# Optimization experiments

Measured on AMD Instinct MI355X. Metric: run time of the kernel, lower is better.

## Reference

```python
import jax, jax.numpy as jnp
import numpy as np

EPS = 1e-12  # F.normalize eps


def setup_inputs() -> dict:
    key = jax.random.key(0)
    k1, k2 = jax.random.split(key)
    bs, d = 8192, 128
    data = jax.random.normal(k1, (bs, d), dtype=jnp.float32)
    label = jax.random.randint(k2, (bs, 1), 0, 2, dtype=jnp.int64)
    scale = jnp.asarray(np.log(1.0 / 0.07), dtype=jnp.float32)  # learned temperature param
    return {"data": data, "scale": scale, "label": label}


def reference(data, scale, label):
    bs = data.shape[0]
    # L2-normalize rows (F.normalize semantics with eps clamp)
    norm = jnp.maximum(jnp.linalg.norm(data, axis=-1, keepdims=True), EPS)
    x = data / norm
    logits = (x @ x.T) * jnp.exp(scale)  # [bs, bs]
    # Vectorized equivalent of the python double loop: binary same-class matrix
    sim = (label == label.T).astype(logits.dtype)  # [bs, bs]
    q = jax.nn.softmax(sim / jnp.sum(sim, axis=-1, keepdims=True), axis=-1)
    p = jax.nn.log_softmax(logits, axis=-1)
    log_q = jnp.log(q)  # q > 0 always (softmax output)
    # F.kl_div(p, q, 'batchmean') = sum(q * (log q - p)) / bs
    loss1 = jnp.sum(q * (log_q - p)) / bs
    # F.kl_div(q.log(), p.exp(), 'batchmean') = sum(exp(p) * (p - log q)) / bs
    loss2 = jnp.sum(jnp.exp(p) * (p - log_q)) / bs
    return (loss1 + loss2) * 0.5
```

## Files before the change

### kernel.cpp

```cpp
#include <hip/hip_runtime.h>
#include <stdint.h>

#define BS 8192
#define DD 128
#define SPLIT 16

typedef __attribute__((ext_vector_type(8))) short short8;
typedef __attribute__((ext_vector_type(4))) float float4v;

__device__ __forceinline__ float bf2f(short s) {
  union { unsigned u; float f; } c;
  c.u = ((unsigned)(unsigned short)s) << 16;
  return c.f;
}
__device__ __forceinline__ short f2bf(float f) {
  union { float f; unsigned u; } c; c.f = f;
  unsigned u = c.u + 0x7FFFu + ((c.u >> 16) & 1u);
  return (short)(u >> 16);
}

__global__ __launch_bounds__(256) void k_norm(const float* __restrict__ data,
                                              const int* __restrict__ label,
                                              unsigned int* __restrict__ xnb32,
                                              float* __restrict__ xnf,
                                              float* __restrict__ gh,
                                              int* __restrict__ cnt,
                                              float* __restrict__ Zr,
                                              float* __restrict__ Ur,
                                              float* __restrict__ Vr,
                                              float* __restrict__ out) {
  __shared__ float sh[256];
  __shared__ int shc[2];
  int tid = threadIdx.x, wave = tid >> 6, lane = tid & 63;
  if (tid < 2) shc[tid] = 0;
  sh[tid] = 0.f;
  if (tid < 32) {
    int row = blockIdx.x * 32 + tid;
    Zr[row] = 0.f; Ur[row] = 0.f; Vr[row] = 0.f;
  }
  if (blockIdx.x == 0 && tid == 0) out[0] = 0.f;
  __syncthreads();
  float a00 = 0.f, a01 = 0.f, a10 = 0.f, a11 = 0.f;
  int c0 = 0, c1 = 0;
  int rbase = blockIdx.x * 32 + wave * 8;
  for (int r = 0; r < 8; ++r) {
    int row = rbase + r;
    float2 v = *(const float2*)&data[row * DD + lane * 2];
    float ss = v.x * v.x + v.y * v.y;
    for (int off = 32; off; off >>= 1) ss += __shfl_xor(ss, off);
    float rn = 1.f / fmaxf(sqrtf(ss), 1e-12f);
    float x0 = v.x * rn, x1 = v.y * rn;
    *(float2*)&xnf[row * DD + lane * 2] = make_float2(x0, x1);
    unsigned int pk = (unsigned int)(unsigned short)f2bf(x0) |
                      ((unsigned int)(unsigned short)f2bf(x1) << 16);
    xnb32[row * 64 + lane] = pk;
    int lab = label[row];
    if (lab == 0) { a00 += x0; a01 += x1; c0++; }
    else          { a10 += x0; a11 += x1; c1++; }
  }
  atomicAdd(&sh[2 * lane], a00);
  atomicAdd(&sh[2 * lane + 1], a01);
  atomicAdd(&sh[128 + 2 * lane], a10);
  atomicAdd(&sh[128 + 2 * lane + 1], a11);
  if (lane == 0) { atomicAdd(&shc[0], c0); atomicAdd(&shc[1], c1); }
  __syncthreads();
  atomicAdd(&gh[tid], sh[tid]);
  if (tid < 2) atomicAdd(&cnt[tid], shc[tid]);
}

__global__ __launch_bounds__(256) void k_main(const unsigned short* __restrict__ xnb,
                                              const int* __restrict__ label,
                                              const float* __restrict__ scale,
                                              float* __restrict__ Zr,
                                              float* __restrict__ Ur,
                                              float* __restrict__ Vr) {
  __shared__ short tile[64 * DD];
  int tid = threadIdx.x, wave = tid >> 6, lane = tid & 63;
  int quad = lane >> 4, col = lane & 15;
  int rb = blockIdx.x / SPLIT, sl = blockIdx.x % SPLIT;
  float se = __expf(scale[0]);

  short8 afrag[2][4];
  int labI[2][4];
#pragma unroll
  for (int s = 0; s < 2; ++s) {
    int arow = rb * 128 + s * 64 + wave * 16 + col;
    const short* ap = (const short*)xnb + (size_t)arow * DD;
#pragma unroll
    for (int t = 0; t < 4; ++t) {
      short8 a = *(const short8*)(ap + t * 32 + quad * 8);
#pragma unroll
      for (int i = 0; i < 8; ++i) a[i] = f2bf(bf2f(a[i]) * se);
      afrag[s][t] = a;
    }
#pragma unroll
    for (int r = 0; r < 4; ++r)
      labI[s][r] = label[rb * 128 + s * 64 + wave * 16 + quad * 4 + r];
  }

  float Z[2][4] = {}, U[2][4] = {}, V0[2][4] = {};

  const char* srcbase = (const char*)xnb;
  int rowloc = tid >> 4;
  int swz = (tid & 15) ^ rowloc;
  for (int j0 = sl * (BS / SPLIT); j0 < (sl + 1) * (BS / SPLIT); j0 += 64) {
    __syncthreads();
    char* dst = ((char*)tile) + tid * 16;
#pragma unroll
    for (int p = 0; p < 4; ++p) {
      const char* src = srcbase + (size_t)(j0 + p * 16 + rowloc) * 256 + swz * 16;
      __builtin_amdgcn_global_load_lds(
          (const __attribute__((address_space(1))) void*)(uintptr_t)src,
          (__attribute__((address_space(3))) void*)(uintptr_t)(dst + p * 4096), 16, 0, 0);
    }
    __syncthreads();
#pragma unroll
    for (int jo = 0; jo < 4; ++jo) {
      int jc = j0 + jo * 16 + col;
      float m0 = (label[jc] == 0) ? 1.f : 0.f;
      float4v c0 = {0.f, 0.f, 0.f, 0.f}, c1 = {0.f, 0.f, 0.f, 0.f};
      const short* bp = tile + (jo * 16 + col) * DD;
#pragma unroll
      for (int t = 0; t < 4; ++t) {
        short8 b = *(const short8*)(bp + ((t * 4 + quad) ^ col) * 8);
        c0 = __builtin_amdgcn_mfma_f32_16x16x32_bf16(afrag[0][t], b, c0, 0, 0, 0);
        c1 = __builtin_amdgcn_mfma_f32_16x16x32_bf16(afrag[1][t], b, c1, 0, 0, 0);
      }
#pragma unroll
      for (int r = 0; r < 4; ++r) {
        float l0 = c0[r], e0 = __expf(l0);
        Z[0][r] += e0; U[0][r] += e0 * l0; V0[0][r] += m0 * e0;
        float l1 = c1[r], e1 = __expf(l1);
        Z[1][r] += e1; U[1][r] += e1 * l1; V0[1][r] += m0 * e1;
      }
    }
  }
#pragma unroll
  for (int s = 0; s < 2; ++s)
#pragma unroll
    for (int r = 0; r < 4; ++r)
#pragma unroll
      for (int off = 1; off < 16; off <<= 1) {
        Z[s][r] += __shfl_xor(Z[s][r], off);
        U[s][r] += __shfl_xor(U[s][r], off);
        V0[s][r] += __shfl_xor(V0[s][r], off);
      }
  if (col == 0) {
#pragma unroll
    for (int s = 0; s < 2; ++s)
#pragma unroll
      for (int r = 0; r < 4; ++r) {
        int row = rb * 128 + s * 64 + wave * 16 + quad * 4 + r;
        float v = (labI[s][r] == 0) ? V0[s][r] : (Z[s][r] - V0[s][r]);
        atomicAdd(&Zr[row], Z[s][r]);
        atomicAdd(&Ur[row], U[s][r]);
        atomicAdd(&Vr[row], v);
      }
  }
}

__global__ __launch_bounds__(256) void k_final(const float* __restrict__ xnf,
                                               const int* __restrict__ label,
                                               const float* __restrict__ scale,
                                               const float* __restrict__ gh,
                                               const int* __restrict__ cnt,
                                               const float* __restrict__ Zr,
                                               const float* __restrict__ Ur,
                                               const float* __restrict__ Vr,
                                               float* __restrict__ out) {
  __shared__ float bsum[4];
  int tid = threadIdx.x, wave = tid >> 6, lane = tid & 63;
  float se = __expf(scale[0]);
  float h0a = gh[2 * lane], h0b = gh[2 * lane + 1];
  float h1a = gh[128 + 2 * lane], h1b = gh[128 + 2 * lane + 1];
  float ga = h0a + h1a, gb = h0b + h1b;
  float c0 = (float)cnt[0], c1 = (float)cnt[1];
  float local = 0.f;
  int rbase = blockIdx.x * 32 + wave * 8;
  for (int r = 0; r < 8; ++r) {
    int row = rbase + r;
    float2 x = *(const float2*)&xnf[row * DD + lane * 2];
    int lab = label[row];
    float sg = x.x * ga + x.y * gb;
    float sh_ = (lab == 0) ? (x.x * h0a + x.y * h0b) : (x.x * h1a + x.y * h1b);
    for (int off = 32; off; off >>= 1) {
      sg += __shfl_xor(sg, off);
      sh_ += __shfl_xor(sh_, off);
    }
    if (lane == 0) {
      float cc = (lab == 0) ? c0 : c1;
      float a = __expf(1.f / cc);
      float Zq = cc * a + ((float)BS - cc);
      float S = se * sg, T = se * sh_;
      float Z = Zr[row], U = Ur[row], V = Vr[row];
      local += a / Zq - (S + (a - 1.f) * T) / Zq + U / Z - V / (cc * Z);
    }
  }
  if (lane == 0) bsum[wave] = local;
  __syncthreads();
  if (tid == 0) {
    float s = bsum[0] + bsum[1] + bsum[2] + bsum[3];
    atomicAdd(out, s * (0.5f / (float)BS));
  }
}

extern "C" void kernel_launch(void* const* d_in, const int* in_sizes, int n_in,
                              void* d_out, int out_size, void* d_ws, size_t ws_size,
                              hipStream_t stream) {
  const float* data = (const float*)d_in[0];
  const float* scale = (const float*)d_in[1];
  const int* label = (const int*)d_in[2];
  char* ws = (char*)d_ws;
  unsigned short* xnb = (unsigned short*)ws;
  unsigned int* xnb32 = (unsigned int*)ws;
  float* xnf = (float*)(ws + 2097152);
  float* Zr = (float*)(ws + 6291456);
  float* Ur = (float*)(ws + 6324224);
  float* Vr = (float*)(ws + 6356992);
  float* gh = (float*)(ws + 6389760);
  int* cnt = (int*)(ws + 6390784);

  hipMemsetAsync(ws + 6389760, 0, 1032, stream);

  k_norm<<<256, 256, 0, stream>>>(data, label, xnb32, xnf, gh, cnt, Zr, Ur, Vr,
                                  (float*)d_out);
  k_main<<<64 * SPLIT, 256, 0, stream>>>(xnb, label, scale, Zr, Ur, Vr);
  k_final<<<256, 256, 0, stream>>>(xnf, label, scale, gh, cnt, Zr, Ur, Vr, (float*)d_out);
}
```

Measured before the change: 125.0 us.

## Load B fragments directly from global, use exp2, and precompute label masks

The main loop no longer stages 64-row tiles into LDS with block-wide barriers. Each wave now reads its B fragments straight from global memory, 16 columns at a time with a 2x unroll, relying on L1/L2 to serve the same rows to all four waves. The exponent moves to base 2 by folding log2(e) into the prescaled A fragments, and the U sum is rescaled by ln2 at the end. A float same-class mask per column is now precomputed in the normalisation kernel instead of comparing labels in the inner loop. This drops the barrier and LDS cost, but each wave now issues its own redundant global loads and depends on cache hit rates.

```diff
diff --git a/kernel.cpp b/kernel.cpp
--- a/kernel.cpp
+++ b/kernel.cpp
@@ -7,6 +7,12 @@
 
 typedef __attribute__((ext_vector_type(8))) short short8;
 typedef __attribute__((ext_vector_type(4))) float float4v;
+
+#if __has_builtin(__builtin_amdgcn_exp2f)
+#define EXP2(x) __builtin_amdgcn_exp2f(x)
+#else
+#define EXP2(x) exp2f(x)
+#endif
 
 __device__ __forceinline__ float bf2f(short s) {
   union { unsigned u; float f; } c;
@@ -28,6 +34,7 @@
                                               float* __restrict__ Zr,
                                               float* __restrict__ Ur,
                                               float* __restrict__ Vr,
+                                              float* __restrict__ mf,
                                               float* __restrict__ out) {
   __shared__ float sh[256];
   __shared__ int shc[2];
@@ -37,6 +44,7 @@
   if (tid < 32) {
     int row = blockIdx.x * 32 + tid;
     Zr[row] = 0.f; Ur[row] = 0.f; Vr[row] = 0.f;
+    mf[row] = (label[row] == 0) ? 1.f : 0.f;
   }
   if (blockIdx.x == 0 && tid == 0) out[0] = 0.f;
   __syncthreads();
@@ -70,15 +78,15 @@
 
 __global__ __launch_bounds__(256) void k_main(const unsigned short* __restrict__ xnb,
                                               const int* __restrict__ label,
+                                              const float* __restrict__ mf,
                                               const float* __restrict__ scale,
                                               float* __restrict__ Zr,
                                               float* __restrict__ Ur,
                                               float* __restrict__ Vr) {
-  __shared__ short tile[64 * DD];
   int tid = threadIdx.x, wave = tid >> 6, lane = tid & 63;
   int quad = lane >> 4, col = lane & 15;
   int rb = blockIdx.x / SPLIT, sl = blockIdx.x % SPLIT;
-  float se = __expf(scale[0]);
+  float se2 = __expf(scale[0]) * 1.4426950408889634f;
 
   short8 afrag[2][4];
   int labI[2][4];
@@ -90,7 +98,7 @@
     for (int t = 0; t < 4; ++t) {
       short8 a = *(const short8*)(ap + t * 32 + quad * 8);
 #pragma unroll
-      for (int i = 0; i < 8; ++i) a[i] = f2bf(bf2f(a[i]) * se);
+      for (int i = 0; i < 8; ++i) a[i] = f2bf(bf2f(a[i]) * se2);
       afrag[s][t] = a;
     }
 #pragma unroll
@@ -100,39 +108,31 @@
 
   float Z[2][4] = {}, U[2][4] = {}, V0[2][4] = {};
 
-  const char* srcbase = (const char*)xnb;
-  int rowloc = tid >> 4;
-  int swz = (tid & 15) ^ rowloc;
-  for (int j0 = sl * (BS / SPLIT); j0 < (sl + 1) * (BS / SPLIT); j0 += 64) {
-    __syncthreads();
-    char* dst = ((char*)tile) + tid * 16;
-#pragma unroll
-    for (int p = 0; p < 4; ++p) {
-      const char* src = srcbase + (size_t)(j0 + p * 16 + rowloc) * 256 + swz * 16;
-      __builtin_amdgcn_global_load_lds(
-          (const __attribute__((address_space(1))) void*)(uintptr_t)src,
-          (__attribute__((address_space(3))) void*)(uintptr_t)(dst + p * 4096), 16, 0, 0);
-    }
-    __syncthreads();
-#pragma unroll
-    for (int jo = 0; jo < 4; ++jo) {
-      int jc = j0 + jo * 16 + col;
-      float m0 = (label[jc] == 0) ? 1.f : 0.f;
-      float4v c0 = {0.f, 0.f, 0.f, 0.f}, c1 = {0.f, 0.f, 0.f, 0.f};
-      const short* bp = tile + (jo * 16 + col) * DD;
-#pragma unroll
-      for (int t = 0; t < 4; ++t) {
-        short8 b = *(const short8*)(bp + ((t * 4 + quad) ^ col) * 8);
-        c0 = __builtin_amdgcn_mfma_f32_16x16x32_bf16(afrag[0][t], b, c0, 0, 0, 0);
-        c1 = __builtin_amdgcn_mfma_f32_16x16x32_bf16(afrag[1][t], b, c1, 0, 0, 0);
-      }
-#pragma unroll
-      for (int r = 0; r < 4; ++r) {
-        float l0 = c0[r], e0 = __expf(l0);
-        Z[0][r] += e0; U[0][r] += e0 * l0; V0[0][r] += m0 * e0;
-        float l1 = c1[r], e1 = __expf(l1);
-        Z[1][r] += e1; U[1][r] += e1 * l1; V0[1][r] += m0 * e1;
-      }
+  const short* xs = (const short*)xnb;
+#pragma unroll 2
+  for (int j0 = sl * (BS / SPLIT); j0 < (sl + 1) * (BS / SPLIT); j0 += 16) {
+    int jc = j0 + col;
+    float m0 = mf[jc];
+    const short* bp = xs + (size_t)jc * DD + quad * 8;
+    short8 b0 = *(const short8*)(bp);
+    short8 b1 = *(const short8*)(bp + 32);
+    short8 b2 = *(const short8*)(bp + 64);
+    short8 b3 = *(const short8*)(bp + 96);
+    float4v c0 = {0.f, 0.f, 0.f, 0.f}, c1 = {0.f, 0.f, 0.f, 0.f};
+    c0 = __builtin_amdgcn_mfma_f32_16x16x32_bf16(afrag[0][0], b0, c0, 0, 0, 0);
+    c1 = __builtin_amdgcn_mfma_f32_16x16x32_bf16(afrag[1][0], b0, c1, 0, 0, 0);
+    c0 = __builtin_amdgcn_mfma_f32_16x16x32_bf16(afrag[0][1], b1, c0, 0, 0, 0);
+    c1 = __builtin_amdgcn_mfma_f32_16x16x32_bf16(afrag[1][1], b1, c1, 0, 0, 0);
+    c0 = __builtin_amdgcn_mfma_f32_16x16x32_bf16(afrag[0][2], b2, c0, 0, 0, 0);
+    c1 = __builtin_amdgcn_mfma_f32_16x16x32_bf16(afrag[1][2], b2, c1, 0, 0, 0);
+    c0 = __builtin_amdgcn_mfma_f32_16x16x32_bf16(afrag[0][3], b3, c0, 0, 0, 0);
+    c1 = __builtin_amdgcn_mfma_f32_16x16x32_bf16(afrag[1][3], b3, c1, 0, 0, 0);
+#pragma unroll
+    for (int r = 0; r < 4; ++r) {
+      float l0 = c0[r], e0 = EXP2(l0);
+      Z[0][r] += e0; U[0][r] += e0 * l0; V0[0][r] += m0 * e0;
+      float l1 = c1[r], e1 = EXP2(l1);
+      Z[1][r] += e1; U[1][r] += e1 * l1; V0[1][r] += m0 * e1;
     }
   }
 #pragma unroll
@@ -153,7 +153,7 @@
         int row = rb * 128 + s * 64 + wave * 16 + quad * 4 + r;
         float v = (labI[s][r] == 0) ? V0[s][r] : (Z[s][r] - V0[s][r]);
         atomicAdd(&Zr[row], Z[s][r]);
-        atomicAdd(&Ur[row], U[s][r]);
+        atomicAdd(&Ur[row], U[s][r] * 0.6931471805599453f);
         atomicAdd(&Vr[row], v);
       }
   }
@@ -219,11 +219,12 @@
   float* Vr = (float*)(ws + 6356992);
   float* gh = (float*)(ws + 6389760);
   int* cnt = (int*)(ws + 6390784);
+  float* mf = (float*)(ws + 6390800);
 
   hipMemsetAsync(ws + 6389760, 0, 1032, stream);
 
-  k_norm<<<256, 256, 0, stream>>>(data, label, xnb32, xnf, gh, cnt, Zr, Ur, Vr,
+  k_norm<<<256, 256, 0, stream>>>(data, label, xnb32, xnf, gh, cnt, Zr, Ur, Vr, mf,
                                   (float*)d_out);
-  k_main<<<64 * SPLIT, 256, 0, stream>>>(xnb, label, scale, Zr, Ur, Vr);
+  k_main<<<64 * SPLIT, 256, 0, stream>>>(xnb, label, mf, scale, Zr, Ur, Vr);
   k_final<<<256, 256, 0, stream>>>(xnf, label, scale, gh, cnt, Zr, Ur, Vr, (float*)d_out);
 }
```

New measurement: 155.5 us. 24.4% more time.

## Double-buffer LDS tiles, use exp2 with pre-scaled logits, precompute label mask

Applied to the files above, without the earlier changes.

Splits the B-tile LDS buffer in two so the global-to-LDS load of the next 64-column tile overlaps the MFMA/exp work on the current one, removing one barrier per tile. It also folds log2(e) into the scaled A fragments so the inner loop uses a native exp2, rescaling U by ln2 at the end. The per-column label compare becomes a precomputed float mask written by k_norm. In exchange, LDS use doubles (32 KB per block), which may lower occupancy, and there is one redundant wrap-around prefetch at the end of the loop.

```diff
diff --git a/kernel.cpp b/kernel.cpp
--- a/kernel.cpp
+++ b/kernel.cpp
@@ -7,6 +7,12 @@
 
 typedef __attribute__((ext_vector_type(8))) short short8;
 typedef __attribute__((ext_vector_type(4))) float float4v;
+
+#if __has_builtin(__builtin_amdgcn_exp2f)
+#define EXP2(x) __builtin_amdgcn_exp2f(x)
+#else
+#define EXP2(x) exp2f(x)
+#endif
 
 __device__ __forceinline__ float bf2f(short s) {
   union { unsigned u; float f; } c;
@@ -28,6 +34,7 @@
                                               float* __restrict__ Zr,
                                               float* __restrict__ Ur,
                                               float* __restrict__ Vr,
+                                              float* __restrict__ mf,
                                               float* __restrict__ out) {
   __shared__ float sh[256];
   __shared__ int shc[2];
@@ -37,6 +44,7 @@
   if (tid < 32) {
     int row = blockIdx.x * 32 + tid;
     Zr[row] = 0.f; Ur[row] = 0.f; Vr[row] = 0.f;
+    mf[row] = (label[row] == 0) ? 1.f : 0.f;
   }
   if (blockIdx.x == 0 && tid == 0) out[0] = 0.f;
   __syncthreads();
@@ -68,17 +76,59 @@
   if (tid < 2) atomicAdd(&cnt[tid], shc[tid]);
 }
 
+__device__ __forceinline__ void stage_tile(const char* srcbase, int j0,
+                                           char* dstbase, int tid) {
+  int rowloc = tid >> 4;
+  int swz = (tid & 15) ^ rowloc;
+  char* dst = dstbase + tid * 16;
+#pragma unroll
+  for (int p = 0; p < 4; ++p) {
+    const char* src = srcbase + (size_t)(j0 + p * 16 + rowloc) * 256 + swz * 16;
+    __builtin_amdgcn_global_load_lds(
+        (const __attribute__((address_space(1))) void*)(uintptr_t)src,
+        (__attribute__((address_space(3))) void*)(uintptr_t)(dst + p * 4096), 16, 0, 0);
+  }
+}
+
+__device__ __forceinline__ void consume_tile(const short* __restrict__ tile, int j0,
+                                             const float* __restrict__ mf,
+                                             const short8 afrag[2][4], int quad, int col,
+                                             float Z[2][4], float U[2][4], float V0[2][4]) {
+#pragma unroll
+  for (int jo = 0; jo < 4; ++jo) {
+    int jc = j0 + jo * 16 + col;
+    float m0 = mf[jc];
+    float4v c0 = {0.f, 0.f, 0.f, 0.f}, c1 = {0.f, 0.f, 0.f, 0.f};
+    const short* bp = tile + (jo * 16 + col) * DD;
+#pragma unroll
+    for (int t = 0; t < 4; ++t) {
+      short8 b = *(const short8*)(bp + ((t * 4 + quad) ^ col) * 8);
+      c0 = __builtin_amdgcn_mfma_f32_16x16x32_bf16(afrag[0][t], b, c0, 0, 0, 0);
+      c1 = __builtin_amdgcn_mfma_f32_16x16x32_bf16(afrag[1][t], b, c1, 0, 0, 0);
+    }
+#pragma unroll
+    for (int r = 0; r < 4; ++r) {
+      float l0 = c0[r], e0 = EXP2(l0);
+      Z[0][r] += e0; U[0][r] += e0 * l0; V0[0][r] += m0 * e0;
+      float l1 = c1[r], e1 = EXP2(l1);
+      Z[1][r] += e1; U[1][r] += e1 * l1; V0[1][r] += m0 * e1;
+    }
+  }
+}
+
 __global__ __launch_bounds__(256) void k_main(const unsigned short* __restrict__ xnb,
                                               const int* __restrict__ label,
+                                              const float* __restrict__ mf,
                                               const float* __restrict__ scale,
                                               float* __restrict__ Zr,
                                               float* __restrict__ Ur,
                                               float* __restrict__ Vr) {
-  __shared__ short tile[64 * DD];
+  __shared__ short tileA[64 * DD];
+  __shared__ short tileB[64 * DD];
   int tid = threadIdx.x, wave = tid >> 6, lane = tid & 63;
   int quad = lane >> 4, col = lane & 15;
   int rb = blockIdx.x / SPLIT, sl = blockIdx.x % SPLIT;
-  float se = __expf(scale[0]);
+  float se2 = __expf(scale[0]) * 1.4426950408889634f;
 
   short8 afrag[2][4];
   int labI[2][4];
@@ -90,7 +140,7 @@
     for (int t = 0; t < 4; ++t) {
       short8 a = *(const short8*)(ap + t * 32 + quad * 8);
 #pragma unroll
-      for (int i = 0; i < 8; ++i) a[i] = f2bf(bf2f(a[i]) * se);
+      for (int i = 0; i < 8; ++i) a[i] = f2bf(bf2f(a[i]) * se2);
       afrag[s][t] = a;
     }
 #pragma unroll
@@ -101,40 +151,20 @@
   float Z[2][4] = {}, U[2][4] = {}, V0[2][4] = {};
 
   const char* srcbase = (const char*)xnb;
-  int rowloc = tid >> 4;
-  int swz = (tid & 15) ^ rowloc;
-  for (int j0 = sl * (BS / SPLIT); j0 < (sl + 1) * (BS / SPLIT); j0 += 64) {
+  int jbase = sl * (BS / SPLIT), jend = jbase + (BS / SPLIT);
+
+  stage_tile(srcbase, jbase, (char*)tileA, tid);
+  __syncthreads();
+  for (int j0 = jbase; j0 < jend; j0 += 128) {
+    stage_tile(srcbase, j0 + 64, (char*)tileB, tid);
+    consume_tile(tileA, j0, mf, afrag, quad, col, Z, U, V0);
     __syncthreads();
-    char* dst = ((char*)tile) + tid * 16;
-#pragma unroll
-    for (int p = 0; p < 4; ++p) {
-      const char* src = srcbase + (size_t)(j0 + p * 16 + rowloc) * 256 + swz * 16;
-      __builtin_amdgcn_global_load_lds(
-          (const __attribute__((address_space(1))) void*)(uintptr_t)src,
-          (__attribute__((address_space(3))) void*)(uintptr_t)(dst + p * 4096), 16, 0, 0);
-    }
+    int jn = (j0 + 128 < jend) ? (j0 + 128) : jbase;
+    stage_tile(srcbase, jn, (char*)tileA, tid);
+    consume_tile(tileB, j0 + 64, mf, afrag, quad, col, Z, U, V0);
     __syncthreads();
-#pragma unroll
-    for (int jo = 0; jo < 4; ++jo) {
-      int jc = j0 + jo * 16 + col;
-      float m0 = (label[jc] == 0) ? 1.f : 0.f;
-      float4v c0 = {0.f, 0.f, 0.f, 0.f}, c1 = {0.f, 0.f, 0.f, 0.f};
-      const short* bp = tile + (jo * 16 + col) * DD;
-#pragma unroll
-      for (int t = 0; t < 4; ++t) {
-        short8 b = *(const short8*)(bp + ((t * 4 + quad) ^ col) * 8);
-        c0 = __builtin_amdgcn_mfma_f32_16x16x32_bf16(afrag[0][t], b, c0, 0, 0, 0);
-        c1 = __builtin_amdgcn_mfma_f32_16x16x32_bf16(afrag[1][t], b, c1, 0, 0, 0);
-      }
-#pragma unroll
-      for (int r = 0; r < 4; ++r) {
-        float l0 = c0[r], e0 = __expf(l0);
-        Z[0][r] += e0; U[0][r] += e0 * l0; V0[0][r] += m0 * e0;
-        float l1 = c1[r], e1 = __expf(l1);
-        Z[1][r] += e1; U[1][r] += e1 * l1; V0[1][r] += m0 * e1;
-      }
-    }
-  }
+  }
+
 #pragma unroll
   for (int s = 0; s < 2; ++s)
 #pragma unroll
@@ -153,7 +183,7 @@
         int row = rb * 128 + s * 64 + wave * 16 + quad * 4 + r;
         float v = (labI[s][r] == 0) ? V0[s][r] : (Z[s][r] - V0[s][r]);
         atomicAdd(&Zr[row], Z[s][r]);
-        atomicAdd(&Ur[row], U[s][r]);
+        atomicAdd(&Ur[row], U[s][r] * 0.6931471805599453f);
         atomicAdd(&Vr[row], v);
       }
   }
@@ -219,11 +249,12 @@
   float* Vr = (float*)(ws + 6356992);
   float* gh = (float*)(ws + 6389760);
   int* cnt = (int*)(ws + 6390784);
+  float* mf = (float*)(ws + 6390800);
 
   hipMemsetAsync(ws + 6389760, 0, 1032, stream);
 
-  k_norm<<<256, 256, 0, stream>>>(data, label, xnb32, xnf, gh, cnt, Zr, Ur, Vr,
+  k_norm<<<256, 256, 0, stream>>>(data, label, xnb32, xnf, gh, cnt, Zr, Ur, Vr, mf,
                                   (float*)d_out);
-  k_main<<<64 * SPLIT, 256, 0, stream>>>(xnb, label, scale, Zr, Ur, Vr);
+  k_main<<<64 * SPLIT, 256, 0, stream>>>(xnb, label, mf, scale, Zr, Ur, Vr);
   k_final<<<256, 256, 0, stream>>>(xnf, label, scale, gh, cnt, Zr, Ur, Vr, (float*)d_out);
 }
```

New measurement: 121.4 us. -2.9%, faster.
